# Kernel tuning notes

Measured on AMD Instinct MI355X. Metric: run time of the kernel, lower is better.

Reference implementation:

```python
import jax, jax.numpy as jnp
import numpy as np

B, T, CH, Hs, Ws = 2, 64, 512, 24, 24
DIM = CH // 2          # 256, attention channel dim
HEADS = 8
HEAD_DIM = DIM // HEADS  # 32
MAX_SEQ = 64


def setup_inputs() -> dict:
    key = jax.random.key(0)
    ks = jax.random.split(key, 6)
    return {
        "x": jax.random.normal(ks[0], (B, T, CH, Hs, Ws), dtype=jnp.float32),
        "rpb_table": jax.random.normal(ks[1], (2 * MAX_SEQ - 1, HEADS), dtype=jnp.float32) * 0.02,
        "qkv_w": jax.random.normal(ks[2], (3 * DIM, DIM), dtype=jnp.float32) * 0.02,
        "qkv_b": jax.random.normal(ks[3], (3 * DIM,), dtype=jnp.float32) * 0.02,
        "proj_w": jax.random.normal(ks[4], (DIM, DIM), dtype=jnp.float32) * 0.02,
        "proj_b": jax.random.normal(ks[5], (DIM,), dtype=jnp.float32) * 0.02,
    }


def reference(x, rpb_table, qkv_w, qkv_b, proj_w, proj_b):
    b, t, c, h, w = x.shape
    half = c // 2
    a_part = x[:, :, :half]       # (B,T,half,H,W) untouched branch
    b_part = x[:, :, half:]       # attention branch

    # 'b t c h w -> (b h w) t c'
    xb = jnp.transpose(b_part, (0, 3, 4, 1, 2)).reshape(b * h * w, t, half)
    B_, N, C = xb.shape
    scale = HEAD_DIM ** -0.5

    qkv = xb @ qkv_w.T + qkv_b                        # (B_, N, 3*C)
    qkv = qkv.reshape(B_, N, 3, HEADS, HEAD_DIM)
    qkv = jnp.transpose(qkv, (2, 0, 3, 1, 4))          # (3, B_, heads, N, hd)
    q, k, v = qkv[0] * scale, qkv[1], qkv[2]

    attn = jnp.einsum('bhnd,bhmd->bhnm', q, k)         # (B_, heads, N, N)

    # relative position bias: index = p2 - p1 + (MAX_SEQ - 1)
    pos = jnp.arange(t)
    rel_idx = pos[None, :] - pos[:, None] + (MAX_SEQ - 1)   # (N, N)
    bias = rpb_table[rel_idx]                              # (N, N, heads)
    bias = jnp.transpose(bias, (2, 0, 1))                  # (heads, N, N)
    attn = attn + bias[None]

    # causal (mask_future=True): -inf strictly above the diagonal
    causal = jnp.where(pos[None, :] > pos[:, None], -jnp.inf, 0.0).astype(attn.dtype)
    attn = attn + causal[None, None]

    attn = jax.nn.softmax(attn, axis=-1)

    out = jnp.einsum('bhnm,bhmd->bhnd', attn, v)       # (B_, heads, N, hd)
    out = jnp.transpose(out, (0, 2, 1, 3)).reshape(B_, N, C)
    out = out @ proj_w.T + proj_b

    # '(b h w) t c -> b t c h w'
    out = out.reshape(b, h, w, t, half)
    out = jnp.transpose(out, (0, 3, 4, 1, 2))

    return jnp.concatenate([a_part, out], axis=2)
```

## Files before the change

### kernel.cpp

```cpp
#include <hip/hip_runtime.h>
#include <hip/hip_bf16.h>

typedef __attribute__((ext_vector_type(4))) float  f32x4;
typedef __attribute__((ext_vector_type(8))) short  bf16x8;
typedef __attribute__((ext_vector_type(8))) unsigned short u16x8;

__device__ __forceinline__ unsigned short f2bf(float f) {
    union { float f; unsigned u; } v; v.f = f;
    unsigned u = v.u;
    unsigned r = u + 0x7fffu + ((u >> 16) & 1u);
    return (unsigned short)(r >> 16);
}


__global__ void cvt_weights(const float* __restrict__ qkv_w, const float* __restrict__ proj_w,
                            unsigned short* __restrict__ wq, unsigned short* __restrict__ wp) {
    int i = blockIdx.x * 256 + threadIdx.x;
    if (i < 196608) wq[i] = f2bf(qkv_w[i]);
    else            wp[i - 196608] = f2bf(proj_w[i - 196608]);
}

__global__ void copy_a(const float* __restrict__ x, float* __restrict__ out) {
    long long i = (long long)blockIdx.x * 256 + threadIdx.x;
    int chunk = (int)(i / 36864);
    int r     = (int)(i % 36864);
    size_t off = (size_t)chunk * 73728 + r;
    ((float4*)out)[off] = ((const float4*)x)[off];
}

__global__ __launch_bounds__(256) void transpose_b(const float* __restrict__ x,
                                                   unsigned short* __restrict__ xb) {
    __shared__ unsigned short tile[256][72];
    const int bt  = blockIdx.x;
    const int hw0 = blockIdx.y * 64;
    const int tid = threadIdx.x;
    const float* src = x + ((size_t)bt * 512 + 256) * 576 + hw0;
    const int c_sub = tid >> 4, l16 = tid & 15;
    #pragma unroll
    for (int it = 0; it < 16; ++it) {
        int cc = it * 16 + c_sub;
        const float4 v = *(const float4*)(src + (size_t)cc * 576 + l16 * 4);
        tile[cc][l16 * 4 + 0] = f2bf(v.x);
        tile[cc][l16 * 4 + 1] = f2bf(v.y);
        tile[cc][l16 * 4 + 2] = f2bf(v.z);
        tile[cc][l16 * 4 + 3] = f2bf(v.w);
    }
    __syncthreads();
    const int row = tid >> 2;
    const int cs  = (tid & 3) * 64;
    const int b = bt >> 6, t = bt & 63;
    size_t m = (size_t)t * 1152 + (size_t)b * 576 + hw0 + row;
    unsigned short* dst = xb + m * 256 + cs;
    #pragma unroll
    for (int q = 0; q < 8; ++q) {
        u16x8 v;
        #pragma unroll
        for (int u = 0; u < 8; ++u) v[u] = tile[cs + q * 8 + u][row];
        *(u16x8*)(dst + q * 8) = v;
    }
}

__global__ __launch_bounds__(256) void gemm_qkv(const unsigned short* __restrict__ A,
                                                const unsigned short* __restrict__ Wt,
                                                const float* __restrict__ bias,
                                                unsigned short* __restrict__ out) {
    __shared__ unsigned short As[128][72];
    __shared__ unsigned short Bs[128][72];
    const int m0 = blockIdx.x * 128, n0 = blockIdx.y * 128;
    const int tid = threadIdx.x;
    const int lane = tid & 63, wid = tid >> 6;
    const int wy = wid >> 1, wx = wid & 1;
    const int c = lane & 15, g = lane >> 4;
    const int srow = tid >> 3, skc = (tid & 7) * 8;
    f32x4 acc[4][4] = {};
    for (int k0 = 0; k0 < 256; k0 += 64) {
        #pragma unroll
        for (int i = 0; i < 4; ++i) {
            int row = srow + 32 * i;
            u16x8 va = *(const u16x8*)(A  + (size_t)(m0 + row) * 256 + k0 + skc);
            *(u16x8*)(&As[row][skc]) = va;
            u16x8 vb = *(const u16x8*)(Wt + (size_t)(n0 + row) * 256 + k0 + skc);
            *(u16x8*)(&Bs[row][skc]) = vb;
        }
        __syncthreads();
        #pragma unroll
        for (int kk = 0; kk < 2; ++kk) {
            bf16x8 af[4], bfg[4];
            #pragma unroll
            for (int mt = 0; mt < 4; ++mt)
                af[mt] = *(const bf16x8*)(&As[wy * 64 + mt * 16 + c][kk * 32 + g * 8]);
            #pragma unroll
            for (int nt = 0; nt < 4; ++nt)
                bfg[nt] = *(const bf16x8*)(&Bs[wx * 64 + nt * 16 + c][kk * 32 + g * 8]);
            #pragma unroll
            for (int mt = 0; mt < 4; ++mt)
                #pragma unroll
                for (int nt = 0; nt < 4; ++nt)
                    acc[mt][nt] = __builtin_amdgcn_mfma_f32_16x16x32_bf16(af[mt], bfg[nt], acc[mt][nt], 0, 0, 0);
        }
        __syncthreads();
    }
    #pragma unroll
    for (int nt = 0; nt < 4; ++nt) {
        int col = n0 + wx * 64 + nt * 16 + c;
        float bv = bias[col];
        #pragma unroll
        for (int mt = 0; mt < 4; ++mt) {
            int row = m0 + wy * 64 + mt * 16 + g * 4;
            #pragma unroll
            for (int r = 0; r < 4; ++r)
                out[(size_t)(row + r) * 768 + col] = f2bf(acc[mt][nt][r] + bv);
        }
    }
}

__global__ __launch_bounds__(64) void attn_kernel(const unsigned short* __restrict__ qkv,
                                                  const float* __restrict__ rpb,
                                                  unsigned short* __restrict__ att) {
    __shared__ float bias_s[127];
    __shared__ unsigned short vT[32][72];
    __shared__ unsigned short P[64][72];
    const int blk = blockIdx.x;
    const int p = blk >> 3, h = blk & 7;
    const int lane = threadIdx.x;
    const int c = lane & 15, g = lane >> 4;

    bias_s[lane] = rpb[lane * 8 + h];
    if (lane < 63) bias_s[64 + lane] = rpb[(64 + lane) * 8 + h];

    {
        const unsigned short* vrow = qkv + (size_t)(lane * 1152 + p) * 768 + 512 + h * 32;
        #pragma unroll
        for (int q = 0; q < 4; ++q) {
            u16x8 v = *(const u16x8*)(vrow + q * 8);
            #pragma unroll
            for (int u = 0; u < 8; ++u) vT[q * 8 + u][lane] = v[u];
        }
    }
    bf16x8 qf[4], kf[4];
    #pragma unroll
    for (int mt = 0; mt < 4; ++mt)
        qf[mt] = *(const bf16x8*)(qkv + (size_t)((mt * 16 + c) * 1152 + p) * 768 + h * 32 + g * 8);
    #pragma unroll
    for (int nt = 0; nt < 4; ++nt)
        kf[nt] = *(const bf16x8*)(qkv + (size_t)((nt * 16 + c) * 1152 + p) * 768 + 256 + h * 32 + g * 8);
    f32x4 s[4][4] = {};
    #pragma unroll
    for (int mt = 0; mt < 4; ++mt)
        #pragma unroll
        for (int nt = 0; nt < 4; ++nt)
            s[mt][nt] = __builtin_amdgcn_mfma_f32_16x16x32_bf16(qf[mt], kf[nt], s[mt][nt], 0, 0, 0);
    __syncthreads();

    const float scale = 0.17677669529663687f;
    #pragma unroll
    for (int mt = 0; mt < 4; ++mt) {
        #pragma unroll
        for (int r = 0; r < 4; ++r) {
            int i = mt * 16 + g * 4 + r;
            float vals[4];
            #pragma unroll
            for (int nt = 0; nt < 4; ++nt) {
                int j = nt * 16 + c;
                float v = s[mt][nt][r] * scale + bias_s[j - i + 63];
                vals[nt] = (j > i) ? -1e30f : v;
            }
            float mx = fmaxf(fmaxf(vals[0], vals[1]), fmaxf(vals[2], vals[3]));
            #pragma unroll
            for (int off = 1; off < 16; off <<= 1) mx = fmaxf(mx, __shfl_xor(mx, off, 64));
            float sum = 0.f;
            #pragma unroll
            for (int nt = 0; nt < 4; ++nt) { vals[nt] = __expf(vals[nt] - mx); sum += vals[nt]; }
            #pragma unroll
            for (int off = 1; off < 16; off <<= 1) sum += __shfl_xor(sum, off, 64);
            float inv = 1.0f / sum;
            #pragma unroll
            for (int nt = 0; nt < 4; ++nt) P[i][nt * 16 + c] = f2bf(vals[nt] * inv);
        }
    }
    __syncthreads();

    f32x4 o[4][2] = {};
    #pragma unroll
    for (int kk = 0; kk < 2; ++kk) {
        bf16x8 pa[4], vb[2];
        #pragma unroll
        for (int mt = 0; mt < 4; ++mt)
            pa[mt] = *(const bf16x8*)(&P[mt * 16 + c][kk * 32 + g * 8]);
        #pragma unroll
        for (int nt = 0; nt < 2; ++nt)
            vb[nt] = *(const bf16x8*)(&vT[nt * 16 + c][kk * 32 + g * 8]);
        #pragma unroll
        for (int mt = 0; mt < 4; ++mt)
            #pragma unroll
            for (int nt = 0; nt < 2; ++nt)
                o[mt][nt] = __builtin_amdgcn_mfma_f32_16x16x32_bf16(pa[mt], vb[nt], o[mt][nt], 0, 0, 0);
    }
    #pragma unroll
    for (int mt = 0; mt < 4; ++mt)
        #pragma unroll
        for (int nt = 0; nt < 2; ++nt) {
            int d = nt * 16 + c;
            #pragma unroll
            for (int r = 0; r < 4; ++r) {
                int i = mt * 16 + g * 4 + r;
                att[(size_t)(i * 1152 + p) * 256 + h * 32 + d] = f2bf(o[mt][nt][r]);
            }
        }
}

__global__ __launch_bounds__(256) void gemm_proj(const unsigned short* __restrict__ A,
                                                 const unsigned short* __restrict__ Wt,
                                                 const float* __restrict__ bias,
                                                 float* __restrict__ out) {
    __shared__ unsigned short As[128][72];
    __shared__ unsigned short Bs[128][72];
    const int m0 = blockIdx.x * 128, n0 = blockIdx.y * 128;
    const int tid = threadIdx.x;
    const int lane = tid & 63, wid = tid >> 6;
    const int wy = wid >> 1, wx = wid & 1;
    const int c = lane & 15, g = lane >> 4;
    const int srow = tid >> 3, skc = (tid & 7) * 8;
    f32x4 acc[4][4] = {};
    for (int k0 = 0; k0 < 256; k0 += 64) {
        #pragma unroll
        for (int i = 0; i < 4; ++i) {
            int row = srow + 32 * i;
            u16x8 va = *(const u16x8*)(A  + (size_t)(m0 + row) * 256 + k0 + skc);
            *(u16x8*)(&As[row][skc]) = va;
            u16x8 vb = *(const u16x8*)(Wt + (size_t)(n0 + row) * 256 + k0 + skc);
            *(u16x8*)(&Bs[row][skc]) = vb;
        }
        __syncthreads();
        #pragma unroll
        for (int kk = 0; kk < 2; ++kk) {
            bf16x8 af[4], bfg[4];
            #pragma unroll
            for (int mt = 0; mt < 4; ++mt)
                af[mt] = *(const bf16x8*)(&As[wy * 64 + mt * 16 + c][kk * 32 + g * 8]);
            #pragma unroll
            for (int nt = 0; nt < 4; ++nt)
                bfg[nt] = *(const bf16x8*)(&Bs[wx * 64 + nt * 16 + c][kk * 32 + g * 8]);
            #pragma unroll
            for (int mt = 0; mt < 4; ++mt)
                #pragma unroll
                for (int nt = 0; nt < 4; ++nt)
                    acc[mt][nt] = __builtin_amdgcn_mfma_f32_16x16x32_bf16(af[mt], bfg[nt], acc[mt][nt], 0, 0, 0);
        }
        __syncthreads();
    }
    #pragma unroll
    for (int nt = 0; nt < 4; ++nt) {
        int col = n0 + wx * 64 + nt * 16 + c;
        float bv = bias[col];
        #pragma unroll
        for (int mt = 0; mt < 4; ++mt) {
            int mbase = m0 + wy * 64 + mt * 16 + g * 4;
            int t   = mbase / 1152;
            int rem = mbase % 1152;
            int b   = rem / 576;
            int hw  = rem % 576;
            float4 v;
            v.x = acc[mt][nt][0] + bv;
            v.y = acc[mt][nt][1] + bv;
            v.z = acc[mt][nt][2] + bv;
            v.w = acc[mt][nt][3] + bv;
            float* dst = out + ((size_t)(b * 64 + t) * 512 + 256 + col) * 576 + hw;
            *(float4*)dst = v;
        }
    }
}

extern "C" void kernel_launch(void* const* d_in, const int* in_sizes, int n_in,
                              void* d_out, int out_size, void* d_ws, size_t ws_size,
                              hipStream_t stream) {
    (void)in_sizes; (void)n_in; (void)out_size;
    const float* x      = (const float*)d_in[0];
    const float* rpb    = (const float*)d_in[1];
    const float* qkv_w  = (const float*)d_in[2];
    const float* qkv_b  = (const float*)d_in[3];
    const float* proj_w = (const float*)d_in[4];
    const float* proj_b = (const float*)d_in[5];
    float* out = (float*)d_out;

    char* ws = (char*)d_ws;
    unsigned short* wq  = (unsigned short*)ws;
    unsigned short* wp  = (unsigned short*)(ws + 393216);
    unsigned short* xb  = (unsigned short*)(ws + 524288);
    unsigned short* qkv = (unsigned short*)(ws + 524288 + 37748736);
    unsigned short* att = xb;
    if (ws_size < (size_t)524288 + 37748736 + 113246208) return;

    cvt_weights<<<1024, 256, 0, stream>>>(qkv_w, proj_w, wq, wp);
    copy_a<<<18432, 256, 0, stream>>>(x, out);
    transpose_b<<<dim3(128, 9), 256, 0, stream>>>(x, xb);
    gemm_qkv<<<dim3(576, 6), 256, 0, stream>>>(xb, wq, qkv_b, qkv);
    attn_kernel<<<9216, 64, 0, stream>>>(qkv, rpb, att);
    gemm_proj<<<dim3(576, 2), 256, 0, stream>>>(att, wp, proj_b, out);
}
```

Before: 240.1 us.

## Use direct global-to-LDS loads with XOR swizzle and swapped operand roles in GEMMs

```diff
diff --git a/kernel.cpp b/kernel.cpp
--- a/kernel.cpp
+++ b/kernel.cpp
@@ -4,12 +4,18 @@
 typedef __attribute__((ext_vector_type(4))) float  f32x4;
 typedef __attribute__((ext_vector_type(8))) short  bf16x8;
 typedef __attribute__((ext_vector_type(8))) unsigned short u16x8;
+typedef __attribute__((ext_vector_type(4))) unsigned short u16x4;
 
 __device__ __forceinline__ unsigned short f2bf(float f) {
     union { float f; unsigned u; } v; v.f = f;
     unsigned u = v.u;
     unsigned r = u + 0x7fffu + ((u >> 16) & 1u);
     return (unsigned short)(r >> 16);
+}
+
+__device__ __forceinline__ void gload16(const void* g, void* l) {
+    __builtin_amdgcn_global_load_lds((const __attribute__((address_space(1))) unsigned*)g,
+                                     (__attribute__((address_space(3))) unsigned*)l, 16, 0, 0);
 }
 
 
@@ -60,56 +66,59 @@
     }
 }
 
-__global__ __launch_bounds__(256) void gemm_qkv(const unsigned short* __restrict__ A,
-                                                const unsigned short* __restrict__ Wt,
-                                                const float* __restrict__ bias,
-                                                unsigned short* __restrict__ out) {
-    __shared__ unsigned short As[128][72];
-    __shared__ unsigned short Bs[128][72];
+__global__ __launch_bounds__(256, 4) void gemm_qkv(const unsigned short* __restrict__ A,
+                                                   const unsigned short* __restrict__ Wt,
+                                                   const float* __restrict__ bias,
+                                                   unsigned short* __restrict__ out) {
+    __shared__ unsigned short Ws[128 * 64];
+    __shared__ unsigned short Xs[128 * 64];
     const int m0 = blockIdx.x * 128, n0 = blockIdx.y * 128;
     const int tid = threadIdx.x;
-    const int lane = tid & 63, wid = tid >> 6;
-    const int wy = wid >> 1, wx = wid & 1;
+    const int lane = tid & 63, w = tid >> 6;
+    const int wy = w >> 1, wx = w & 1;
     const int c = lane & 15, g = lane >> 4;
-    const int srow = tid >> 3, skc = (tid & 7) * 8;
+    const int lr = lane >> 3, lu = lane & 7;
+    const int su = lu ^ lr;
+    const int cs7 = c & 7;
     f32x4 acc[4][4] = {};
     for (int k0 = 0; k0 < 256; k0 += 64) {
         #pragma unroll
-        for (int i = 0; i < 4; ++i) {
-            int row = srow + 32 * i;
-            u16x8 va = *(const u16x8*)(A  + (size_t)(m0 + row) * 256 + k0 + skc);
-            *(u16x8*)(&As[row][skc]) = va;
-            u16x8 vb = *(const u16x8*)(Wt + (size_t)(n0 + row) * 256 + k0 + skc);
-            *(u16x8*)(&Bs[row][skc]) = vb;
+        for (int q = 0; q < 4; ++q) {
+            int R = w * 32 + q * 8;
+            gload16(Wt + (size_t)(n0 + R + lr) * 256 + k0 + su * 8, &Ws[R * 64]);
+            gload16(A  + (size_t)(m0 + R + lr) * 256 + k0 + su * 8, &Xs[R * 64]);
         }
         __syncthreads();
         #pragma unroll
         for (int kk = 0; kk < 2; ++kk) {
-            bf16x8 af[4], bfg[4];
-            #pragma unroll
-            for (int mt = 0; mt < 4; ++mt)
-                af[mt] = *(const bf16x8*)(&As[wy * 64 + mt * 16 + c][kk * 32 + g * 8]);
-            #pragma unroll
-            for (int nt = 0; nt < 4; ++nt)
-                bfg[nt] = *(const bf16x8*)(&Bs[wx * 64 + nt * 16 + c][kk * 32 + g * 8]);
-            #pragma unroll
-            for (int mt = 0; mt < 4; ++mt)
+            bf16x8 af[4], bx[4];
+            #pragma unroll
+            for (int a2 = 0; a2 < 4; ++a2)
+                af[a2] = *(const bf16x8*)(&Ws[(wy * 64 + a2 * 16 + c) * 64 + (((kk * 4 + g) ^ cs7) * 8)]);
+            #pragma unroll
+            for (int b2 = 0; b2 < 4; ++b2)
+                bx[b2] = *(const bf16x8*)(&Xs[(wx * 64 + b2 * 16 + c) * 64 + (((kk * 4 + g) ^ cs7) * 8)]);
+            #pragma unroll
+            for (int a2 = 0; a2 < 4; ++a2)
                 #pragma unroll
-                for (int nt = 0; nt < 4; ++nt)
-                    acc[mt][nt] = __builtin_amdgcn_mfma_f32_16x16x32_bf16(af[mt], bfg[nt], acc[mt][nt], 0, 0, 0);
+                for (int b2 = 0; b2 < 4; ++b2)
+                    acc[a2][b2] = __builtin_amdgcn_mfma_f32_16x16x32_bf16(af[a2], bx[b2], acc[a2][b2], 0, 0, 0);
         }
         __syncthreads();
     }
     #pragma unroll
-    for (int nt = 0; nt < 4; ++nt) {
-        int col = n0 + wx * 64 + nt * 16 + c;
-        float bv = bias[col];
-        #pragma unroll
-        for (int mt = 0; mt < 4; ++mt) {
-            int row = m0 + wy * 64 + mt * 16 + g * 4;
-            #pragma unroll
-            for (int r = 0; r < 4; ++r)
-                out[(size_t)(row + r) * 768 + col] = f2bf(acc[mt][nt][r] + bv);
+    for (int a2 = 0; a2 < 4; ++a2) {
+        int n = n0 + wy * 64 + a2 * 16 + g * 4;
+        float4 bv = *(const float4*)(bias + n);
+        #pragma unroll
+        for (int b2 = 0; b2 < 4; ++b2) {
+            int m = m0 + wx * 64 + b2 * 16 + c;
+            u16x4 v;
+            v[0] = f2bf(acc[a2][b2][0] + bv.x);
+            v[1] = f2bf(acc[a2][b2][1] + bv.y);
+            v[2] = f2bf(acc[a2][b2][2] + bv.z);
+            v[3] = f2bf(acc[a2][b2][3] + bv.w);
+            *(u16x4*)(out + (size_t)m * 768 + n) = v;
         }
     }
 }
@@ -209,64 +218,62 @@
         }
 }
 
-__global__ __launch_bounds__(256) void gemm_proj(const unsigned short* __restrict__ A,
-                                                 const unsigned short* __restrict__ Wt,
-                                                 const float* __restrict__ bias,
-                                                 float* __restrict__ out) {
-    __shared__ unsigned short As[128][72];
-    __shared__ unsigned short Bs[128][72];
+__global__ __launch_bounds__(256, 4) void gemm_proj(const unsigned short* __restrict__ A,
+                                                    const unsigned short* __restrict__ Wt,
+                                                    const float* __restrict__ bias,
+                                                    float* __restrict__ out) {
+    __shared__ unsigned short Ws[128 * 64];
+    __shared__ unsigned short Xs[128 * 64];
     const int m0 = blockIdx.x * 128, n0 = blockIdx.y * 128;
     const int tid = threadIdx.x;
-    const int lane = tid & 63, wid = tid >> 6;
-    const int wy = wid >> 1, wx = wid & 1;
+    const int lane = tid & 63, w = tid >> 6;
+    const int wy = w >> 1, wx = w & 1;
     const int c = lane & 15, g = lane >> 4;
-    const int srow = tid >> 3, skc = (tid & 7) * 8;
+    const int lr = lane >> 3, lu = lane & 7;
+    const int su = lu ^ lr;
+    const int cs7 = c & 7;
     f32x4 acc[4][4] = {};
     for (int k0 = 0; k0 < 256; k0 += 64) {
         #pragma unroll
-        for (int i = 0; i < 4; ++i) {
-            int row = srow + 32 * i;
-            u16x8 va = *(const u16x8*)(A  + (size_t)(m0 + row) * 256 + k0 + skc);
-            *(u16x8*)(&As[row][skc]) = va;
-            u16x8 vb = *(const u16x8*)(Wt + (size_t)(n0 + row) * 256 + k0 + skc);
-            *(u16x8*)(&Bs[row][skc]) = vb;
+        for (int q = 0; q < 4; ++q) {
+            int R = w * 32 + q * 8;
+            gload16(Wt + (size_t)(n0 + R + lr) * 256 + k0 + su * 8, &Ws[R * 64]);
+            gload16(A  + (size_t)(m0 + R + lr) * 256 + k0 + su * 8, &Xs[R * 64]);
         }
         __syncthreads();
         #pragma unroll
         for (int kk = 0; kk < 2; ++kk) {
-            bf16x8 af[4], bfg[4];
-            #pragma unroll
-            for (int mt = 0; mt < 4; ++mt)
-                af[mt] = *(const bf16x8*)(&As[wy * 64 + mt * 16 + c][kk * 32 + g * 8]);
-            #pragma unroll
-            for (int nt = 0; nt < 4; ++nt)
-                bfg[nt] = *(const bf16x8*)(&Bs[wx * 64 + nt * 16 + c][kk * 32 + g * 8]);
-            #pragma unroll
-            for (int mt = 0; mt < 4; ++mt)
+            bf16x8 af[4], bx[4];
+            #pragma unroll
+            for (int a2 = 0; a2 < 4; ++a2)
+                af[a2] = *(const bf16x8*)(&Ws[(wy * 64 + a2 * 16 + c) * 64 + (((kk * 4 + g) ^ cs7) * 8)]);
+            #pragma unroll
+            for (int b2 = 0; b2 < 4; ++b2)
+                bx[b2] = *(const bf16x8*)(&Xs[(wx * 64 + b2 * 16 + c) * 64 + (((kk * 4 + g) ^ cs7) * 8)]);
+            #pragma unroll
+            for (int a2 = 0; a2 < 4; ++a2)
                 #pragma unroll
-                for (int nt = 0; nt < 4; ++nt)
-                    acc[mt][nt] = __builtin_amdgcn_mfma_f32_16x16x32_bf16(af[mt], bfg[nt], acc[mt][nt], 0, 0, 0);
+                for (int b2 = 0; b2 < 4; ++b2)
+                    acc[a2][b2] = __builtin_amdgcn_mfma_f32_16x16x32_bf16(af[a2], bx[b2], acc[a2][b2], 0, 0, 0);
         }
         __syncthreads();
     }
     #pragma unroll
-    for (int nt = 0; nt < 4; ++nt) {
-        int col = n0 + wx * 64 + nt * 16 + c;
-        float bv = bias[col];
-        #pragma unroll
-        for (int mt = 0; mt < 4; ++mt) {
-            int mbase = m0 + wy * 64 + mt * 16 + g * 4;
-            int t   = mbase / 1152;
-            int rem = mbase % 1152;
-            int b   = rem / 576;
+    for (int a2 = 0; a2 < 4; ++a2) {
+        int n = n0 + wy * 64 + a2 * 16 + g * 4;
+        float4 bv = *(const float4*)(bias + n);
+        #pragma unroll
+        for (int b2 = 0; b2 < 4; ++b2) {
+            int m = m0 + wx * 64 + b2 * 16 + c;
+            int t   = m / 1152;
+            int rem = m % 1152;
+            int bb  = rem / 576;
             int hw  = rem % 576;
-            float4 v;
-            v.x = acc[mt][nt][0] + bv;
-            v.y = acc[mt][nt][1] + bv;
-            v.z = acc[mt][nt][2] + bv;
-            v.w = acc[mt][nt][3] + bv;
-            float* dst = out + ((size_t)(b * 64 + t) * 512 + 256 + col) * 576 + hw;
-            *(float4*)dst = v;
+            float* dst = out + ((size_t)(bb * 64 + t) * 512 + 256 + n) * 576 + hw;
+            dst[0]        = acc[a2][b2][0] + bv.x;
+            dst[576]      = acc[a2][b2][1] + bv.y;
+            dst[2 * 576]  = acc[a2][b2][2] + bv.z;
+            dst[3 * 576]  = acc[a2][b2][3] + bv.w;
         }
     }
 }
```

After: 225.8 us. -6.0%, faster.
